# Performance work log

Measured on AMD Instinct MI355X. Metric: run time of the kernel, lower is better.

Reference implementation:

```python
import jax, jax.numpy as jnp
import numpy as np

TOL = 1e-7  # tolerant_zero_error
HID = 32


def _gcn_layer(x, a, W, b):
    # spektral-style GCNConv: relu(A_norm @ X @ W + b)
    return jax.nn.relu(jnp.einsum('bnm,bmf->bnf', a, x @ W) + b)


def setup_inputs() -> dict:
    key = jax.random.key(0)
    ks = jax.random.split(key, 12)
    B, N, F = 8, 2048, 64
    x = jax.random.normal(ks[0], (B, N, F), dtype=jnp.float32)
    a = jax.random.uniform(ks[1], (B, N, N), dtype=jnp.float32)
    def he(k, shape):
        fan_in = shape[0]
        lim = jnp.sqrt(6.0 / fan_in)
        return jax.random.uniform(k, shape, jnp.float32, -lim, lim)
    return {
        'x': x, 'a': a,
        'W1': he(ks[2], (F, HID)),   'b1': jnp.zeros((HID,), jnp.float32),
        'W2': he(ks[3], (HID, HID)), 'b2': jnp.zeros((HID,), jnp.float32),
        'W3': he(ks[4], (HID, HID)), 'b3': jnp.zeros((HID,), jnp.float32),
        'Wf1': he(ks[5], (HID, 2 * HID)), 'bf1': jnp.zeros((2 * HID,), jnp.float32),
        'Wf2': he(ks[6], (2 * HID, 1)),   'bf2': jnp.zeros((1,), jnp.float32),
    }


def reference(x, a, W1, b1, W2, b2, W3, b3, Wf1, bf1, Wf2, bf2):
    x = x.astype(jnp.float32)
    a = a.astype(jnp.float32)
    B, N, _ = a.shape
    # add_self_loop: put 1 on diagonal entries whose current value is ~0
    diag = jnp.diagonal(a, axis1=-2, axis2=-1)            # [B,N]
    add = jnp.where(jnp.abs(diag) < TOL, 1.0, 0.0)        # [B,N]
    eye = jnp.eye(N, dtype=a.dtype)
    a = a + add[:, :, None] * eye
    # norm_a: D^-1/2 A D^-1/2 (diag matmuls == elementwise d_i * a_ij * d_j)
    d = jnp.sum(a, axis=-1)                               # [B,N]
    dm = d ** -0.5
    a = dm[:, :, None] * a * dm[:, None, :]
    # GCNConv stack
    h = _gcn_layer(x, a, W1, b1)
    h = _gcn_layer(h, a, W2, b2)
    h = _gcn_layer(h, a, W3, b3)
    # GlobalMaxPool over nodes
    g = jnp.max(h, axis=1)                                # [B,HID]
    # MLP head
    g = jax.nn.relu(g @ Wf1 + bf1)
    out = g @ Wf2 + bf2                                   # [B,1]
    return out
```

## Files before the change

### kernel.cpp

```cpp
#include <hip/hip_runtime.h>

#define BB 8
#define NN 2048
#define FF 64
#define HH 32
#define CK 128
#define NCHK (NN / CK)

typedef __attribute__((ext_vector_type(8))) short short8;
typedef __attribute__((ext_vector_type(4))) float floatx4;

static __device__ __forceinline__ float warp_sum64(float v) {
  for (int off = 32; off; off >>= 1) v += __shfl_down(v, off, 64);
  return v;
}

static __device__ __forceinline__ unsigned int f2bf_rne(float f) {
  unsigned int u = __float_as_uint(f);
  return (u + 0x7fffu + ((u >> 16) & 1u)) >> 16;
}
static __device__ __forceinline__ float bf2f(unsigned short s) {
  return __uint_as_float(((unsigned int)s) << 16);
}

#define GLOAD_LDS16(g, l)                                                 \
  __builtin_amdgcn_global_load_lds(                                       \
      (const __attribute__((address_space(1))) unsigned int*)(g),         \
      (__attribute__((address_space(3))) unsigned int*)(l), 16, 0, 0)

__global__ __launch_bounds__(256) void deg_cvt_kernel(const float* __restrict__ A,
                                                      float* __restrict__ dm,
                                                      float* __restrict__ addf,
                                                      unsigned short* __restrict__ Abf) {
  const int lane = threadIdx.x & 63;
  const int w = threadIdx.x >> 6;
  const size_t row = (size_t)blockIdx.x * 4 + w;
  const size_t n = row & (NN - 1);
  const float* Ar = A + row * (size_t)NN;
  unsigned int* Abr = (unsigned int*)(Abf + row * (size_t)NN);
  float sum = 0.f;
#pragma unroll
  for (int it = 0; it < 8; ++it) {
    float4 v = *(const float4*)(Ar + it * 256 + lane * 4);
    sum += v.x + v.y + v.z + v.w;
    uint2 p;
    p.x = f2bf_rne(v.x) | (f2bf_rne(v.y) << 16);
    p.y = f2bf_rne(v.z) | (f2bf_rne(v.w) << 16);
    *(uint2*)(Abr + it * 128 + lane * 2) = p;
  }
  sum = warp_sum64(sum);
  if (lane == 0) {
    const float diag = Ar[n];
    const float ad = (fabsf(diag) < 1e-7f) ? 1.f : 0.f;
    dm[row] = 1.f / sqrtf(sum + ad);
    addf[row] = ad;
  }
}

__global__ __launch_bounds__(256) void xw_kernel(const float* __restrict__ x,
                                                 const float* __restrict__ W1,
                                                 const float* __restrict__ dm,
                                                 unsigned short* __restrict__ hst) {
  __shared__ float xs[8][FF + 1];
  __shared__ float wl[FF * HH];
  const int tid = threadIdx.x;
  const size_t row0 = (size_t)blockIdx.x * 8;
  for (int k = tid; k < FF * HH; k += 256) wl[k] = W1[k];
  for (int k = tid; k < 8 * FF; k += 256) xs[k >> 6][k & 63] = x[row0 * FF + k];
  __syncthreads();
  const int r = tid >> 5, c = tid & 31;
  float acc = 0.f;
#pragma unroll
  for (int k = 0; k < FF; ++k) acc = fmaf(xs[r][k], wl[k * HH + c], acc);
  const size_t row = row0 + r;
  const int b = (int)(row >> 11);
  const int n = (int)(row & (NN - 1));
  hst[((size_t)b * HH + c) * NN + n] = (unsigned short)f2bf_rne(dm[row] * acc);
}

__global__ __launch_bounds__(64) void layer_kernel(const unsigned short* __restrict__ Abf,
                                                   const unsigned short* __restrict__ hst_in,
                                                   const float* __restrict__ dm,
                                                   const float* __restrict__ addf,
                                                   const float* __restrict__ bias,
                                                   const float* __restrict__ Wn,
                                                   unsigned short* __restrict__ hst_next,
                                                   unsigned int* __restrict__ gmax,
                                                   const int do_pool) {
  __shared__ __align__(16) unsigned char smem[3][12288];

  const int tid = threadIdx.x;
  const int mb = blockIdx.x & 127;
  const int b = blockIdx.x >> 7;
  const int mrow0 = mb * 16;
  const int q = tid >> 4;
  const int l15 = tid & 15;

  const unsigned short* aSrc[4];
  const unsigned short* bSrc[8];
#pragma unroll
  for (int i = 0; i < 4; ++i) {
    const int r = i * 4 + q;
    const int gl = l15 ^ r;
    aSrc[i] = Abf + ((size_t)(b * NN + mrow0 + r)) * NN + gl * 8;
  }
#pragma unroll
  for (int i = 0; i < 8; ++i) {
    const int r = i * 4 + q;
    const int gl = l15 ^ (r & 15);
    bSrc[i] = hst_in + ((size_t)(b * HH + r)) * NN + gl * 8;
  }

#define ISSUE(buf)                                                        \
  do {                                                                    \
    _Pragma("unroll") for (int i = 0; i < 4; ++i) {                       \
      GLOAD_LDS16(aSrc[i], &smem[buf][i * 1024]);                         \
      aSrc[i] += CK;                                                      \
    }                                                                     \
    _Pragma("unroll") for (int i = 0; i < 8; ++i) {                       \
      GLOAD_LDS16(bSrc[i], &smem[buf][4096 + i * 1024]);                  \
      bSrc[i] += CK;                                                      \
    }                                                                     \
  } while (0)

  floatx4 acc0 = {0.f, 0.f, 0.f, 0.f};
  floatx4 acc1 = {0.f, 0.f, 0.f, 0.f};

  ISSUE(0);
  ISSUE(1);
#pragma unroll
  for (int c = 0; c < NCHK; ++c) {
    if (c + 2 < NCHK) ISSUE((c + 2) % 3);
    if (c <= NCHK - 3) {
      asm volatile("s_waitcnt vmcnt(24)" ::: "memory");
    } else if (c == NCHK - 2) {
      asm volatile("s_waitcnt vmcnt(12)" ::: "memory");
    } else {
      asm volatile("s_waitcnt vmcnt(0)" ::: "memory");
    }
    const unsigned char* Ab = smem[c % 3];
    const unsigned char* Bb = smem[c % 3] + 4096;
#pragma unroll
    for (int ks = 0; ks < 4; ++ks) {
      const int go = (((ks * 4 + q) ^ l15) * 16);
      short8 af = *(const short8*)(Ab + l15 * 256 + go);
      short8 b0 = *(const short8*)(Bb + l15 * 256 + go);
      short8 b1 = *(const short8*)(Bb + 4096 + l15 * 256 + go);
      acc0 = __builtin_amdgcn_mfma_f32_16x16x32_bf16(af, b0, acc0, 0, 0, 0);
      acc1 = __builtin_amdgcn_mfma_f32_16x16x32_bf16(af, b1, acc1, 0, 0, 0);
    }
  }
#undef ISSUE

  float h0[4], h1[4];
#pragma unroll
  for (int r = 0; r < 4; ++r) {
    const int row = q * 4 + r;
    const int rg = b * NN + mrow0 + row;
    const float dmv = dm[rg], adv = addf[rg];
    const float hs0 = bf2f(hst_in[((size_t)b * HH + l15) * NN + mrow0 + row]);
    const float hs1 = bf2f(hst_in[((size_t)b * HH + 16 + l15) * NN + mrow0 + row]);
    h0[r] = fmaxf(fmaf(dmv, acc0[r] + adv * hs0, bias[l15]), 0.f);
    h1[r] = fmaxf(fmaf(dmv, acc1[r] + adv * hs1, bias[16 + l15]), 0.f);
  }

  if (do_pool) {
    float m0 = fmaxf(fmaxf(h0[0], h0[1]), fmaxf(h0[2], h0[3]));
    float m1 = fmaxf(fmaxf(h1[0], h1[1]), fmaxf(h1[2], h1[3]));
    m0 = fmaxf(m0, __shfl_xor(m0, 16, 64));
    m0 = fmaxf(m0, __shfl_xor(m0, 32, 64));
    m1 = fmaxf(m1, __shfl_xor(m1, 16, 64));
    m1 = fmaxf(m1, __shfl_xor(m1, 32, 64));
    if (q == 0) {
      atomicMax(&gmax[b * HH + l15], __float_as_uint(m0));
      atomicMax(&gmax[b * HH + 16 + l15], __float_as_uint(m1));
    }
  } else {
    float* hb = (float*)&smem[0][0];
    __syncthreads();
#pragma unroll
    for (int r = 0; r < 4; ++r) {
      const int row = q * 4 + r;
      hb[row * 33 + l15] = h0[r];
      hb[row * 33 + 16 + l15] = h1[r];
    }
    __syncthreads();
    unsigned short o0[4], o1[4];
#pragma unroll
    for (int r = 0; r < 4; ++r) {
      const int row = q * 4 + r;
      const int rg = b * NN + mrow0 + row;
      float s0 = 0.f, s1 = 0.f;
#pragma unroll
      for (int k = 0; k < HH; ++k) {
        const float hv = hb[row * 33 + k];
        s0 = fmaf(hv, Wn[k * HH + l15], s0);
        s1 = fmaf(hv, Wn[k * HH + 16 + l15], s1);
      }
      const float dmv = dm[rg];
      o0[r] = (unsigned short)f2bf_rne(dmv * s0);
      o1[r] = (unsigned short)f2bf_rne(dmv * s1);
    }
    *(ushort4*)(hst_next + ((size_t)b * HH + l15) * NN + mrow0 + q * 4) =
        *(ushort4*)o0;
    *(ushort4*)(hst_next + ((size_t)b * HH + 16 + l15) * NN + mrow0 + q * 4) =
        *(ushort4*)o1;
  }
}

__global__ __launch_bounds__(64) void head_kernel(const unsigned int* __restrict__ gmax,
                                                  const float* __restrict__ Wf1,
                                                  const float* __restrict__ bf1,
                                                  const float* __restrict__ Wf2,
                                                  const float* __restrict__ bf2,
                                                  float* __restrict__ out) {
  const int b = blockIdx.x;
  const int t = threadIdx.x;
  float acc = bf1[t];
#pragma unroll
  for (int c = 0; c < HH; ++c)
    acc = fmaf(__uint_as_float(gmax[b * HH + c]), Wf1[c * (2 * HH) + t], acc);
  acc = fmaxf(acc, 0.f);
  float v = acc * Wf2[t];
  v = warp_sum64(v);
  if (t == 0) out[b] = v + bf2[0];
}

extern "C" void kernel_launch(void* const* d_in, const int* in_sizes, int n_in,
                              void* d_out, int out_size, void* d_ws, size_t ws_size,
                              hipStream_t stream) {
  const float* x   = (const float*)d_in[0];
  const float* a   = (const float*)d_in[1];
  const float* W1  = (const float*)d_in[2];
  const float* b1  = (const float*)d_in[3];
  const float* W2  = (const float*)d_in[4];
  const float* b2  = (const float*)d_in[5];
  const float* W3  = (const float*)d_in[6];
  const float* b3  = (const float*)d_in[7];
  const float* Wf1 = (const float*)d_in[8];
  const float* bf1 = (const float*)d_in[9];
  const float* Wf2 = (const float*)d_in[10];
  const float* bf2 = (const float*)d_in[11];
  float* out = (float*)d_out;

  float* ws = (float*)d_ws;
  const size_t BN = (size_t)BB * NN;
  float* dm   = ws;
  float* addf = dm + BN;
  unsigned int* gmax = (unsigned int*)(addf + BN);
  unsigned short* hst_a = (unsigned short*)(gmax + 256);
  unsigned short* hst_b = hst_a + BN * HH;
  unsigned short* Abf = hst_b + BN * HH;

  hipMemsetAsync(gmax, 0, BB * HH * sizeof(unsigned int), stream);

  deg_cvt_kernel<<<BN / 4, 256, 0, stream>>>(a, dm, addf, Abf);
  xw_kernel<<<BN / 8, 256, 0, stream>>>(x, W1, dm, hst_a);

  layer_kernel<<<BB * 128, 64, 0, stream>>>(Abf, hst_a, dm, addf, b1, W2, hst_b, nullptr, 0);
  layer_kernel<<<BB * 128, 64, 0, stream>>>(Abf, hst_b, dm, addf, b2, W3, hst_a, nullptr, 0);
  layer_kernel<<<BB * 128, 64, 0, stream>>>(Abf, hst_a, dm, addf, b3, nullptr, nullptr, gmax, 1);

  head_kernel<<<BB, 64, 0, stream>>>(gmax, Wf1, bf1, Wf2, bf2, out);
}
```

Baseline: 279.2 us.

## Fuse degree/bf16 conversion with X@W1 and gmax init into one kernel

Merges the degree/bf16 conversion kernel, the x@W1 kernel and the gmax memset into a single kernel. This removes two launches and the dm round trip through global memory. Adjacency and x reads are now nontemporal loads. The layer epilogue now reads dm, addf and hst_in with vectorized float4/ushort4 loads instead of scalar per-row loads. In exchange, every block of the big A-streaming kernel also loads all of W1 into LDS, which adds redundant traffic and uses more LDS.

```diff
diff --git a/kernel.cpp b/kernel.cpp
--- a/kernel.cpp
+++ b/kernel.cpp
@@ -15,6 +15,11 @@
   return v;
 }
 
+static __device__ __forceinline__ float warp_bsum64(float v) {
+  for (int off = 1; off < 64; off <<= 1) v += __shfl_xor(v, off, 64);
+  return v;
+}
+
 static __device__ __forceinline__ unsigned int f2bf_rne(float f) {
   unsigned int u = __float_as_uint(f);
   return (u + 0x7fffu + ((u >> 16) & 1u)) >> 16;
@@ -28,54 +33,58 @@
       (const __attribute__((address_space(1))) unsigned int*)(g),         \
       (__attribute__((address_space(3))) unsigned int*)(l), 16, 0, 0)
 
-__global__ __launch_bounds__(256) void deg_cvt_kernel(const float* __restrict__ A,
-                                                      float* __restrict__ dm,
-                                                      float* __restrict__ addf,
-                                                      unsigned short* __restrict__ Abf) {
-  const int lane = threadIdx.x & 63;
-  const int w = threadIdx.x >> 6;
+__global__ __launch_bounds__(256) void deg_cvt_xw_kernel(
+    const float* __restrict__ A, const float* __restrict__ x,
+    const float* __restrict__ W1, float* __restrict__ dm,
+    float* __restrict__ addf, unsigned short* __restrict__ Abf,
+    unsigned short* __restrict__ hst, unsigned int* __restrict__ gmax) {
+  __shared__ float wl[FF * HH];
+  __shared__ float xs[4][FF];
+  const int tid = threadIdx.x;
+  const int lane = tid & 63;
+  const int w = tid >> 6;
   const size_t row = (size_t)blockIdx.x * 4 + w;
   const size_t n = row & (NN - 1);
+  const int b = (int)(row >> 11);
+
+  if (blockIdx.x == 0) gmax[tid] = 0;
+
+  for (int k = tid; k < FF * HH; k += 256) wl[k] = W1[k];
+  xs[w][lane] = __builtin_nontemporal_load(x + row * FF + lane);
+
   const float* Ar = A + row * (size_t)NN;
   unsigned int* Abr = (unsigned int*)(Abf + row * (size_t)NN);
   float sum = 0.f;
 #pragma unroll
   for (int it = 0; it < 8; ++it) {
-    float4 v = *(const float4*)(Ar + it * 256 + lane * 4);
+    floatx4 v = __builtin_nontemporal_load(
+        (const floatx4*)(Ar + it * 256 + lane * 4));
     sum += v.x + v.y + v.z + v.w;
     uint2 p;
     p.x = f2bf_rne(v.x) | (f2bf_rne(v.y) << 16);
     p.y = f2bf_rne(v.z) | (f2bf_rne(v.w) << 16);
     *(uint2*)(Abr + it * 128 + lane * 2) = p;
   }
-  sum = warp_sum64(sum);
+  sum = warp_bsum64(sum);
+  const float diag = Ar[n];
+  const float ad = (fabsf(diag) < 1e-7f) ? 1.f : 0.f;
+  const float dmv = 1.f / sqrtf(sum + ad);
   if (lane == 0) {
-    const float diag = Ar[n];
-    const float ad = (fabsf(diag) < 1e-7f) ? 1.f : 0.f;
-    dm[row] = 1.f / sqrtf(sum + ad);
+    dm[row] = dmv;
     addf[row] = ad;
   }
-}
-
-__global__ __launch_bounds__(256) void xw_kernel(const float* __restrict__ x,
-                                                 const float* __restrict__ W1,
-                                                 const float* __restrict__ dm,
-                                                 unsigned short* __restrict__ hst) {
-  __shared__ float xs[8][FF + 1];
-  __shared__ float wl[FF * HH];
-  const int tid = threadIdx.x;
-  const size_t row0 = (size_t)blockIdx.x * 8;
-  for (int k = tid; k < FF * HH; k += 256) wl[k] = W1[k];
-  for (int k = tid; k < 8 * FF; k += 256) xs[k >> 6][k & 63] = x[row0 * FF + k];
+
   __syncthreads();
-  const int r = tid >> 5, c = tid & 31;
+  const int c = lane & 31, h = lane >> 5;
   float acc = 0.f;
 #pragma unroll
-  for (int k = 0; k < FF; ++k) acc = fmaf(xs[r][k], wl[k * HH + c], acc);
-  const size_t row = row0 + r;
-  const int b = (int)(row >> 11);
-  const int n = (int)(row & (NN - 1));
-  hst[((size_t)b * HH + c) * NN + n] = (unsigned short)f2bf_rne(dm[row] * acc);
+  for (int k = 0; k < 32; ++k) {
+    const int kk = h * 32 + k;
+    acc = fmaf(xs[w][kk], wl[kk * HH + c], acc);
+  }
+  acc += __shfl_down(acc, 32, 64);
+  if (lane < 32)
+    hst[((size_t)b * HH + c) * NN + n] = (unsigned short)f2bf_rne(dmv * acc);
 }
 
 __global__ __launch_bounds__(64) void layer_kernel(const unsigned short* __restrict__ Abf,
@@ -152,14 +161,19 @@
   }
 #undef ISSUE
 
+  const float4 dmq = *(const float4*)(dm + b * NN + mrow0 + q * 4);
+  const float4 adq = *(const float4*)(addf + b * NN + mrow0 + q * 4);
+  const ushort4 hv0 =
+      *(const ushort4*)(hst_in + ((size_t)b * HH + l15) * NN + mrow0 + q * 4);
+  const ushort4 hv1 =
+      *(const ushort4*)(hst_in + ((size_t)b * HH + 16 + l15) * NN + mrow0 + q * 4);
   float h0[4], h1[4];
 #pragma unroll
   for (int r = 0; r < 4; ++r) {
-    const int row = q * 4 + r;
-    const int rg = b * NN + mrow0 + row;
-    const float dmv = dm[rg], adv = addf[rg];
-    const float hs0 = bf2f(hst_in[((size_t)b * HH + l15) * NN + mrow0 + row]);
-    const float hs1 = bf2f(hst_in[((size_t)b * HH + 16 + l15) * NN + mrow0 + row]);
+    const float dmv = ((const float*)&dmq)[r];
+    const float adv = ((const float*)&adq)[r];
+    const float hs0 = bf2f(((const unsigned short*)&hv0)[r]);
+    const float hs1 = bf2f(((const unsigned short*)&hv1)[r]);
     h0[r] = fmaxf(fmaf(dmv, acc0[r] + adv * hs0, bias[l15]), 0.f);
     h1[r] = fmaxf(fmaf(dmv, acc1[r] + adv * hs1, bias[16 + l15]), 0.f);
   }
@@ -252,10 +266,7 @@
   unsigned short* hst_b = hst_a + BN * HH;
   unsigned short* Abf = hst_b + BN * HH;
 
-  hipMemsetAsync(gmax, 0, BB * HH * sizeof(unsigned int), stream);
-
-  deg_cvt_kernel<<<BN / 4, 256, 0, stream>>>(a, dm, addf, Abf);
-  xw_kernel<<<BN / 8, 256, 0, stream>>>(x, W1, dm, hst_a);
+  deg_cvt_xw_kernel<<<BN / 4, 256, 0, stream>>>(a, x, W1, dm, addf, Abf, hst_a, gmax);
 
   layer_kernel<<<BB * 128, 64, 0, stream>>>(Abf, hst_a, dm, addf, b1, W2, hst_b, nullptr, 0);
   layer_kernel<<<BB * 128, 64, 0, stream>>>(Abf, hst_b, dm, addf, b2, W3, hst_a, nullptr, 0);
```

Measured after the change: 258.1 us. 7.6% less time.
